# Kernel optimization log

Measured on AMD Instinct MI355X. Metric: run time of the kernel, lower is better.

## Reference

```python
import jax, jax.numpy as jnp
import numpy as np

B, S, D, H, O = 256, 64, 256, 1024, 512
N_CELLS = 3


def setup_inputs() -> dict:
    key = jax.random.key(0)
    ks = jax.random.split(key, 16)

    def u(k, shape, fan):
        return (jax.random.uniform(k, shape, jnp.float32, -1.0, 1.0) / np.float32(np.sqrt(fan)))

    inp = {"inputs": jax.random.normal(ks[0], (B, S, D), jnp.float32)}
    in_dims = [D, H, H]
    i = 1
    for c in range(N_CELLS):
        inp[f"w_ih_{c}"] = u(ks[i], (3 * H, in_dims[c]), H); i += 1
        inp[f"w_hh_{c}"] = u(ks[i], (3 * H, H), H); i += 1
        inp[f"b_ih_{c}"] = u(ks[i], (3 * H,), H); i += 1
        inp[f"b_hh_{c}"] = u(ks[i], (3 * H,), H); i += 1
    inp["lin_w"] = u(ks[13], (S, H, O), H)   # per-step linear weights (same_linear=False)
    inp["lin_b"] = u(ks[14], (S, O), H)
    return inp


def _gru_cell(x, h, w_ih, w_hh, b_ih, b_hh):
    # PyTorch GRUCell gate order: r, z, n
    gi = x @ w_ih.T + b_ih          # [B, 3H]
    gh = h @ w_hh.T + b_hh          # [B, 3H]
    i_r, i_z, i_n = jnp.split(gi, 3, axis=-1)
    h_r, h_z, h_n = jnp.split(gh, 3, axis=-1)
    r = jax.nn.sigmoid(i_r + h_r)
    z = jax.nn.sigmoid(i_z + h_z)
    n = jnp.tanh(i_n + r * h_n)
    return (1.0 - z) * n + z * h


def reference(inputs, w_ih_0, w_hh_0, b_ih_0, b_hh_0,
              w_ih_1, w_hh_1, b_ih_1, b_hh_1,
              w_ih_2, w_hh_2, b_ih_2, b_hh_2,
              lin_w, lin_b):
    params = [(w_ih_0, w_hh_0, b_ih_0, b_hh_0),
              (w_ih_1, w_hh_1, b_ih_1, b_hh_1),
              (w_ih_2, w_hh_2, b_ih_2, b_hh_2)]
    batch = inputs.shape[0]
    hdim = w_hh_0.shape[1]

    def step(hs, xs):
        x_t, wL, bL = xs              # [B,D], [H,O], [O]
        new_hs = []
        cur = x_t
        for i, (wi, wh, bi, bh) in enumerate(params):
            h = _gru_cell(cur, hs[i], wi, wh, bi, bh)
            new_hs.append(h)
            cur = h
        out = cur @ wL + bL           # [B,O]
        return tuple(new_hs), out

    h0 = tuple(jnp.zeros((batch, hdim), inputs.dtype) for _ in range(N_CELLS))
    xs = (jnp.swapaxes(inputs, 0, 1), lin_w, lin_b)  # scan over seq dim
    hs, outs = jax.lax.scan(step, h0, xs)            # outs: [S,B,O]
    return (jnp.swapaxes(outs, 0, 1), hs[0], hs[1], hs[2])
```

## Files before the change

kernel.cpp:

```cpp
#include <hip/hip_runtime.h>
#include <hip/hip_bf16.h>
#include <stdint.h>

#define B_ 256
#define S_ 64
#define D_ 256
#define H_ 1024
#define O_ 512
#define G_ 3072
#define BH_ (B_ * H_)
#define RING_ 32

typedef unsigned short u16;
typedef __attribute__((ext_vector_type(8))) short bf16x8;
typedef __attribute__((ext_vector_type(4))) float f32x4;

#define MFMA16(a, b, c) __builtin_amdgcn_mfma_f32_16x16x32_bf16((a), (b), (c), 0, 0, 0)

__device__ __forceinline__ u16 f2b(float f) {
    union { float f; uint32_t u; } v; v.f = f;
    uint32_t u = v.u;
    return (u16)((u + 0x7fffu + ((u >> 16) & 1u)) >> 16);
}

__device__ __forceinline__ void gl_lds16(const u16* g, u16* l) {
    __builtin_amdgcn_global_load_lds(
        (const __attribute__((address_space(1))) unsigned int*)g,
        (__attribute__((address_space(3))) unsigned int*)l, 16, 0, 0);
}
__device__ __forceinline__ unsigned long long sysld64(const u16* p) {
    return __hip_atomic_load((const unsigned long long*)p, __ATOMIC_RELAXED, __HIP_MEMORY_SCOPE_SYSTEM);
}
__device__ __forceinline__ void sysst64(u16* p, unsigned long long v) {
    __hip_atomic_store((unsigned long long*)p, v, __ATOMIC_RELAXED, __HIP_MEMORY_SCOPE_SYSTEM);
}
__device__ __forceinline__ void waitflag(int* f, int n) {
    while (__hip_atomic_load(f, __ATOMIC_RELAXED, __HIP_MEMORY_SCOPE_SYSTEM) < n)
        __builtin_amdgcn_s_sleep(8);
    asm volatile("" ::: "memory");
}
__device__ __forceinline__ void postflag(int* f) {
    __hip_atomic_fetch_add(f, 1, __ATOMIC_RELAXED, __HIP_MEMORY_SCOPE_SYSTEM);
}


__global__ void k_conv(const float* __restrict__ s, u16* __restrict__ d, int n4) {
    int i = blockIdx.x * blockDim.x + threadIdx.x;
    int st = gridDim.x * blockDim.x;
    for (; i < n4; i += st) {
        float4 v = ((const float4*)s)[i];
        ushort4 o;
        o.x = f2b(v.x); o.y = f2b(v.y); o.z = f2b(v.z); o.w = f2b(v.w);
        ((ushort4*)d)[i] = o;
    }
}

__global__ __launch_bounds__(256) void k_twl(const float* __restrict__ w, u16* __restrict__ o) {
    __shared__ float tile[32][33];
    int bid = blockIdx.x;
    int t = bid >> 9;
    int rem = bid & 511;
    int j0 = (rem >> 4) << 5;
    int o0 = (rem & 15) << 5;
    int tx = threadIdx.x & 31, ty = threadIdx.x >> 5;
    const float* base = w + (size_t)t * (H_ * O_);
#pragma unroll
    for (int i = 0; i < 4; ++i) {
        int r = ty + (i << 3);
        tile[r][tx] = base[(size_t)(j0 + r) * O_ + o0 + tx];
    }
    __syncthreads();
    u16* ob = o + (size_t)t * (O_ * H_);
#pragma unroll
    for (int i = 0; i < 4; ++i) {
        int r = ty + (i << 3);
        ob[(size_t)(o0 + r) * H_ + j0 + tx] = f2b(tile[tx][r]);
    }
}


struct GruArgs {
    const u16* Xb;
    const u16 *Wi0, *Wh0, *Wi1, *Wh1, *Wi2, *Wh2;
    const float *bi0, *bh0, *bi1, *bh1, *bi2, *bh2;
    u16 *h0, *h1, *h2a;
    const u16* WLt;
    const float* lb;
    float* out;
    int* ready;
    int* consumed;
};

__global__ __launch_bounds__(512, 1) void k_gru(GruArgs p) {
    __shared__ u16 Wb[2][3][128 * 64];
    __shared__ u16 Ab[2][32 * 64];
    __shared__ float carry[32 * 132];

    const int w = blockIdx.x;
    const int xcd = w & 7;
    const int slot = w >> 3;
    const int role = slot >> 3;
    const int sub = slot & 7;
    const int b0 = sub * 32;

    const int tid = threadIdx.x;
    const int wid = tid >> 6, lane = tid & 63;
    const int fr = lane & 15, kc = lane >> 4;

    const int arow = tid >> 4;
    const int acol = (tid & 15) << 2;
    const int adst = arow * 64 + ((((tid & 15) >> 1) ^ (arow & 7)) << 3) + ((tid & 1) << 2);

    int sw0 = ((kc ^ (fr & 7)) << 3);
    int sw1 = (((4 + kc) ^ (fr & 7)) << 3);

    int* ready = p.ready;
    int* consumed = p.consumed;

    for (int i = tid; i < 32 * 132; i += 512) carry[i] = 0.f;
    __syncthreads();

    if (role < 3) {
        const u16 *Wi, *Wh; const float *bi, *bh; int K0;
        if (role == 0)      { Wi = p.Wi0; Wh = p.Wh0; bi = p.bi0; bh = p.bh0; K0 = D_; }
        else if (role == 1) { Wi = p.Wi1; Wh = p.Wh1; bi = p.bi1; bh = p.bh1; K0 = H_; }
        else                { Wi = p.Wi2; Wh = p.Wh2; bi = p.bi2; bh = p.bh2; K0 = H_; }
        const int nXc = K0 >> 6;
        const int nC = nXc + 16;
        const int j0 = xcd * 128;
        const int jme = j0 + (wid << 4) + fr;
        const float b_r = bi[jme] + bh[jme];
        const float b_z = bi[H_ + jme] + bh[H_ + jme];
        const float b_i = bi[2 * H_ + jme];
        const float b_h = bh[2 * H_ + jme];

        const u16 *A0 = nullptr, *Ah = nullptr; int ld0 = H_;
        u16* hout = nullptr;

        auto LA = [&](int c) -> unsigned long long {
            const u16* s = (c < nXc) ? (A0 + (size_t)arow * ld0 + (c << 6) + acol)
                                     : (Ah + (size_t)arow * H_ + ((c - nXc) << 6) + acol);
            return sysld64(s);
        };
        auto SW = [&](int c, int nb) {
            if (c < nXc) {
                int ko = c << 6;
#pragma unroll
                for (int hh = 0; hh < 2; ++hh) {
                    int ci = (hh << 9) + tid, jr = ci >> 3, c8 = ci & 7;
                    size_t ro = (size_t)(j0 + jr) * K0 + ko + ((c8 ^ (jr & 7)) << 3);
                    gl_lds16(Wi + ro,                       &Wb[nb][0][ci << 3]);
                    gl_lds16(Wi + (size_t)H_ * K0 + ro,     &Wb[nb][1][ci << 3]);
                    gl_lds16(Wi + (size_t)2 * H_ * K0 + ro, &Wb[nb][2][ci << 3]);
                }
            } else {
                int ko = (c - nXc) << 6;
#pragma unroll
                for (int hh = 0; hh < 2; ++hh) {
                    int ci = (hh << 9) + tid, jr = ci >> 3, c8 = ci & 7;
                    size_t ro = (size_t)(j0 + jr) * H_ + ko + ((c8 ^ (jr & 7)) << 3);
                    gl_lds16(Wh + ro,                       &Wb[nb][0][ci << 3]);
                    gl_lds16(Wh + (size_t)H_ * H_ + ro,     &Wb[nb][1][ci << 3]);
                    gl_lds16(Wh + (size_t)2 * H_ * H_ + ro, &Wb[nb][2][ci << 3]);
                }
            }
        };

        for (int t = 0; t < S_; ++t) {
            if (role == 0) {
                if (t) waitflag(&ready[0 * 64 + t - 1], 64);
                A0 = p.Xb + (size_t)b0 * (S_ * D_) + t * D_; ld0 = S_ * D_;
                Ah = p.h0 + (size_t)((t + RING_ - 1) & (RING_ - 1)) * BH_ + (size_t)b0 * H_;
                hout = p.h0 + (size_t)(t & (RING_ - 1)) * BH_;
            } else if (role == 1) {
                waitflag(&ready[0 * 64 + t], 64);
                if (t) waitflag(&ready[1 * 64 + t - 1], 64);
                A0 = p.h0 + (size_t)(t & (RING_ - 1)) * BH_ + (size_t)b0 * H_; ld0 = H_;
                Ah = p.h1 + (size_t)((t + RING_ - 1) & (RING_ - 1)) * BH_ + (size_t)b0 * H_;
                hout = p.h1 + (size_t)(t & (RING_ - 1)) * BH_;
            } else {
                waitflag(&ready[1 * 64 + t], 64);
                if (t) waitflag(&ready[2 * 64 + t - 1], 64);
                A0 = p.h1 + (size_t)(t & (RING_ - 1)) * BH_ + (size_t)b0 * H_; ld0 = H_;
                Ah = p.h2a + (size_t)t * BH_ + (size_t)b0 * H_;
                hout = p.h2a + (size_t)(t + 1) * BH_;
            }

            f32x4 accR[2] = {}, accZ[2] = {}, accI[2] = {}, accN[2] = {};

            unsigned long long la0 = LA(0), la1 = LA(1);
            *(unsigned long long*)&Ab[0][adst] = la0;
            SW(0, 0);
            la0 = LA(2);

            auto BODY = [&](int s, unsigned long long& laReg) {
                if (s + 2 < nC) asm volatile("s_waitcnt vmcnt(1)" ::: "memory");
                else            asm volatile("s_waitcnt vmcnt(0)" ::: "memory");
                asm volatile("s_waitcnt lgkmcnt(0)" ::: "memory");
                __builtin_amdgcn_s_barrier();
                __builtin_amdgcn_sched_barrier(0);
                if (s + 1 < nC) {
                    *(unsigned long long*)&Ab[(s + 1) & 1][adst] = laReg;
                    SW(s + 1, (s + 1) & 1);
                }
                if (s + 3 < nC) laReg = LA(s + 3);
                const int cur = s & 1;
                const int bo = ((wid << 4) + fr) * 64;
                bf16x8 a00 = *(const bf16x8*)&Ab[cur][fr * 64 + sw0];
                bf16x8 a01 = *(const bf16x8*)&Ab[cur][fr * 64 + sw1];
                bf16x8 a10 = *(const bf16x8*)&Ab[cur][(16 + fr) * 64 + sw0];
                bf16x8 a11 = *(const bf16x8*)&Ab[cur][(16 + fr) * 64 + sw1];
                bf16x8 r0 = *(const bf16x8*)&Wb[cur][0][bo + sw0];
                bf16x8 r1 = *(const bf16x8*)&Wb[cur][0][bo + sw1];
                bf16x8 z0 = *(const bf16x8*)&Wb[cur][1][bo + sw0];
                bf16x8 z1 = *(const bf16x8*)&Wb[cur][1][bo + sw1];
                bf16x8 q0 = *(const bf16x8*)&Wb[cur][2][bo + sw0];
                bf16x8 q1 = *(const bf16x8*)&Wb[cur][2][bo + sw1];
                __builtin_amdgcn_s_setprio(1);
                accR[0] = MFMA16(a00, r0, accR[0]); accR[0] = MFMA16(a01, r1, accR[0]);
                accR[1] = MFMA16(a10, r0, accR[1]); accR[1] = MFMA16(a11, r1, accR[1]);
                accZ[0] = MFMA16(a00, z0, accZ[0]); accZ[0] = MFMA16(a01, z1, accZ[0]);
                accZ[1] = MFMA16(a10, z0, accZ[1]); accZ[1] = MFMA16(a11, z1, accZ[1]);
                if (s < nXc) {
                    accI[0] = MFMA16(a00, q0, accI[0]); accI[0] = MFMA16(a01, q1, accI[0]);
                    accI[1] = MFMA16(a10, q0, accI[1]); accI[1] = MFMA16(a11, q1, accI[1]);
                } else {
                    accN[0] = MFMA16(a00, q0, accN[0]); accN[0] = MFMA16(a01, q1, accN[0]);
                    accN[1] = MFMA16(a10, q0, accN[1]); accN[1] = MFMA16(a11, q1, accN[1]);
                }
                __builtin_amdgcn_s_setprio(0);
            };
            for (int s = 0; s < nC; s += 2) { BODY(s, la1); BODY(s + 1, la0); }

            if (role <= 1 && t >= RING_) waitflag(&consumed[role * 64 + (t - RING_)], 128);

            u16* hrep = &Wb[0][0][0];
#pragma unroll
            for (int m = 0; m < 2; ++m)
#pragma unroll
                for (int i = 0; i < 4; ++i) {
                    int row = m * 16 + kc * 4 + i;
                    float rv = 1.f / (1.f + __expf(-(accR[m][i] + b_r)));
                    float zv = 1.f / (1.f + __expf(-(accZ[m][i] + b_z)));
                    float nv = tanhf(accI[m][i] + b_i + rv * (accN[m][i] + b_h));
                    float hp = carry[row * 132 + (wid << 4) + fr];
                    float hn = (1.f - zv) * nv + zv * hp;
                    carry[row * 132 + (wid << 4) + fr] = hn;
                    hrep[row * 128 + (wid << 4) + fr] = f2b(hn);
                }
            __syncthreads();
            {
                int rr = tid >> 4, jo = (tid & 15) << 3;
                unsigned long long v0 = *(const unsigned long long*)&hrep[rr * 128 + jo];
                unsigned long long v1 = *(const unsigned long long*)&hrep[rr * 128 + jo + 4];
                u16* dst = hout + (size_t)(b0 + rr) * H_ + j0 + jo;
                sysst64(dst, v0);
                sysst64(dst + 4, v1);
            }
            if (t == S_ - 1) {
                int rr = tid >> 4, jo = (tid & 15) << 3;
                float* od = p.out + (size_t)B_ * S_ * O_ + (size_t)role * BH_ +
                            (size_t)(b0 + rr) * H_ + j0 + jo;
                *(float4*)od       = *(const float4*)&carry[rr * 132 + jo];
                *(float4*)(od + 4) = *(const float4*)&carry[rr * 132 + jo + 4];
            }
            asm volatile("s_waitcnt vmcnt(0)" ::: "memory");
            __syncthreads();
            if (tid == 0) {
                postflag(&ready[role * 64 + t]);
                if (role == 0) { if (t) postflag(&consumed[0 * 64 + t - 1]); }
                else if (role == 1) {
                    postflag(&consumed[0 * 64 + t]);
                    if (t) postflag(&consumed[1 * 64 + t - 1]);
                } else {
                    postflag(&consumed[1 * 64 + t]);
                }
            }
            __syncthreads();
        }
    } else {
        const int o0 = xcd << 6;
        const int nC = 16;
        const int mg = wid >> 2, og = wid & 3;
        const u16 *A0 = nullptr, *Wl = nullptr;

        auto LAl = [&](int c) -> unsigned long long {
            return sysld64(A0 + (size_t)arow * H_ + (c << 6) + acol);
        };
        auto SWl = [&](int c, int nb) {
            int orow = tid >> 3, c8 = tid & 7;
            gl_lds16(Wl + (size_t)(o0 + orow) * H_ + (c << 6) + ((c8 ^ (orow & 7)) << 3),
                     &Wb[nb][0][tid << 3]);
        };

        for (int t = 0; t < S_; ++t) {
            waitflag(&ready[2 * 64 + t], 64);
            A0 = p.h2a + (size_t)(t + 1) * BH_ + (size_t)b0 * H_;
            Wl = p.WLt + (size_t)t * (O_ * H_);

            f32x4 acc = {0.f, 0.f, 0.f, 0.f};
            unsigned long long la0 = LAl(0), la1 = LAl(1);
            *(unsigned long long*)&Ab[0][adst] = la0;
            SWl(0, 0);
            la0 = LAl(2);

            auto BODYL = [&](int s, unsigned long long& laReg) {
                if (s + 2 < nC) asm volatile("s_waitcnt vmcnt(1)" ::: "memory");
                else            asm volatile("s_waitcnt vmcnt(0)" ::: "memory");
                asm volatile("s_waitcnt lgkmcnt(0)" ::: "memory");
                __builtin_amdgcn_s_barrier();
                __builtin_amdgcn_sched_barrier(0);
                if (s + 1 < nC) {
                    *(unsigned long long*)&Ab[(s + 1) & 1][adst] = laReg;
                    SWl(s + 1, (s + 1) & 1);
                }
                if (s + 3 < nC) laReg = LAl(s + 3);
                const int cur = s & 1;
                bf16x8 a0 = *(const bf16x8*)&Ab[cur][(mg * 16 + fr) * 64 + sw0];
                bf16x8 a1 = *(const bf16x8*)&Ab[cur][(mg * 16 + fr) * 64 + sw1];
                bf16x8 w0 = *(const bf16x8*)&Wb[cur][0][(og * 16 + fr) * 64 + sw0];
                bf16x8 w1 = *(const bf16x8*)&Wb[cur][0][(og * 16 + fr) * 64 + sw1];
                __builtin_amdgcn_s_setprio(1);
                acc = MFMA16(a0, w0, acc);
                acc = MFMA16(a1, w1, acc);
                __builtin_amdgcn_s_setprio(0);
            };
            for (int s = 0; s < nC; s += 2) { BODYL(s, la1); BODYL(s + 1, la0); }

            float bb = p.lb[t * O_ + o0 + og * 16 + fr];
#pragma unroll
            for (int i = 0; i < 4; ++i) {
                int row = mg * 16 + kc * 4 + i;
                p.out[((size_t)(b0 + row) * S_ + t) * O_ + o0 + og * 16 + fr] = acc[i] + bb;
            }
        }
    }
}


extern "C" void kernel_launch(void* const* d_in, const int* in_sizes, int n_in,
                              void* d_out, int out_size, void* d_ws, size_t ws_size,
                              hipStream_t stream) {
    (void)in_sizes; (void)n_in; (void)out_size; (void)ws_size;
    const float* x   = (const float*)d_in[0];
    const float* wi0 = (const float*)d_in[1];
    const float* wh0 = (const float*)d_in[2];
    const float* bi0 = (const float*)d_in[3];
    const float* bh0 = (const float*)d_in[4];
    const float* wi1 = (const float*)d_in[5];
    const float* wh1 = (const float*)d_in[6];
    const float* bi1 = (const float*)d_in[7];
    const float* bh1 = (const float*)d_in[8];
    const float* wi2 = (const float*)d_in[9];
    const float* wh2 = (const float*)d_in[10];
    const float* bi2 = (const float*)d_in[11];
    const float* bh2 = (const float*)d_in[12];
    const float* lw  = (const float*)d_in[13];
    const float* lb  = (const float*)d_in[14];

    char* base = (char*)d_ws;
    size_t off = 0;
    auto alloc = [&](size_t bytes) {
        char* p = base + off;
        off = (off + bytes + 255) & ~(size_t)255;
        return p;
    };
    u16* Xb  = (u16*)alloc((size_t)B_ * S_ * D_ * 2);
    u16* Wi0 = (u16*)alloc((size_t)G_ * D_ * 2);
    u16* Wh0 = (u16*)alloc((size_t)G_ * H_ * 2);
    u16* Wi1 = (u16*)alloc((size_t)G_ * H_ * 2);
    u16* Wh1 = (u16*)alloc((size_t)G_ * H_ * 2);
    u16* Wi2 = (u16*)alloc((size_t)G_ * H_ * 2);
    u16* Wh2 = (u16*)alloc((size_t)G_ * H_ * 2);
    u16* h0  = (u16*)alloc((size_t)RING_ * BH_ * 2);
    u16* h1  = (u16*)alloc((size_t)RING_ * BH_ * 2);
    u16* h2a = (u16*)alloc((size_t)(S_ + 1) * BH_ * 2);
    u16* WLt = (u16*)alloc((size_t)S_ * O_ * H_ * 2);
    int* flags = (int*)alloc((size_t)(3 * 64 + 2 * 64) * 4);
    int* ready = flags;
    int* consumed = flags + 3 * 64;

    k_conv<<<1024, 256, 0, stream>>>(x,   Xb,  (B_ * S_ * D_) / 4);
    k_conv<<<1024, 256, 0, stream>>>(wi0, Wi0, (G_ * D_) / 4);
    k_conv<<<1024, 256, 0, stream>>>(wh0, Wh0, (G_ * H_) / 4);
    k_conv<<<1024, 256, 0, stream>>>(wi1, Wi1, (G_ * H_) / 4);
    k_conv<<<1024, 256, 0, stream>>>(wh1, Wh1, (G_ * H_) / 4);
    k_conv<<<1024, 256, 0, stream>>>(wi2, Wi2, (G_ * H_) / 4);
    k_conv<<<1024, 256, 0, stream>>>(wh2, Wh2, (G_ * H_) / 4);
    k_twl<<<S_ * 512, 256, 0, stream>>>(lw, WLt);
    hipMemsetAsync(h0 + (size_t)(RING_ - 1) * BH_, 0, (size_t)BH_ * 2, stream);
    hipMemsetAsync(h1 + (size_t)(RING_ - 1) * BH_, 0, (size_t)BH_ * 2, stream);
    hipMemsetAsync(h2a, 0, (size_t)BH_ * 2, stream);
    hipMemsetAsync(flags, 0, (size_t)(3 * 64 + 2 * 64) * 4, stream);

    GruArgs ga;
    ga.Xb = Xb;
    ga.Wi0 = Wi0; ga.Wh0 = Wh0; ga.Wi1 = Wi1; ga.Wh1 = Wh1; ga.Wi2 = Wi2; ga.Wh2 = Wh2;
    ga.bi0 = bi0; ga.bh0 = bh0; ga.bi1 = bi1; ga.bh1 = bh1; ga.bi2 = bi2; ga.bh2 = bh2;
    ga.h0 = h0; ga.h1 = h1; ga.h2a = h2a;
    ga.WLt = WLt; ga.lb = lb; ga.out = (float*)d_out;
    ga.ready = ready; ga.consumed = consumed;

    void* args[] = {&ga};
    hipLaunchCooperativeKernel((void*)k_gru, dim3(256), dim3(512), args, 0, stream);
}
```

Measured before the change: 2.615 ms.

## Triple-buffer weight tiles, use sc0 sc1 loads, keep hidden carry in registers

```diff
diff --git a/kernel.cpp b/kernel.cpp
--- a/kernel.cpp
+++ b/kernel.cpp
@@ -28,11 +28,15 @@
         (const __attribute__((address_space(1))) unsigned int*)g,
         (__attribute__((address_space(3))) unsigned int*)l, 16, 0, 0);
 }
-__device__ __forceinline__ unsigned long long sysld64(const u16* p) {
-    return __hip_atomic_load((const unsigned long long*)p, __ATOMIC_RELAXED, __HIP_MEMORY_SCOPE_SYSTEM);
-}
-__device__ __forceinline__ void sysst64(u16* p, unsigned long long v) {
-    __hip_atomic_store((unsigned long long*)p, v, __ATOMIC_RELAXED, __HIP_MEMORY_SCOPE_SYSTEM);
+__device__ __forceinline__ unsigned long long gld_sys(const u16* p) {
+    unsigned long long v;
+    asm volatile("global_load_dwordx2 %0, %1, off sc0 sc1"
+                 : "=v"(v) : "v"(p) : "memory");
+    return v;
+}
+__device__ __forceinline__ void gst_sys(u16* p, unsigned long long v) {
+    asm volatile("global_store_dwordx2 %0, %1, off sc0 sc1"
+                 :: "v"(p), "v"(v) : "memory");
 }
 __device__ __forceinline__ void waitflag(int* f, int n) {
     while (__hip_atomic_load(f, __ATOMIC_RELAXED, __HIP_MEMORY_SCOPE_SYSTEM) < n)
@@ -92,9 +96,8 @@
 };
 
 __global__ __launch_bounds__(512, 1) void k_gru(GruArgs p) {
-    __shared__ u16 Wb[2][3][128 * 64];
+    __shared__ u16 Wb[3][3][128 * 64];
     __shared__ u16 Ab[2][32 * 64];
-    __shared__ float carry[32 * 132];
 
     const int w = blockIdx.x;
     const int xcd = w & 7;
@@ -116,9 +119,6 @@
 
     int* ready = p.ready;
     int* consumed = p.consumed;
-
-    for (int i = tid; i < 32 * 132; i += 512) carry[i] = 0.f;
-    __syncthreads();
 
     if (role < 3) {
         const u16 *Wi, *Wh; const float *bi, *bh; int K0;
@@ -137,10 +137,12 @@
         const u16 *A0 = nullptr, *Ah = nullptr; int ld0 = H_;
         u16* hout = nullptr;
 
+        f32x4 hcar[2] = {};
+
         auto LA = [&](int c) -> unsigned long long {
             const u16* s = (c < nXc) ? (A0 + (size_t)arow * ld0 + (c << 6) + acol)
                                      : (Ah + (size_t)arow * H_ + ((c - nXc) << 6) + acol);
-            return sysld64(s);
+            return gld_sys(s);
         };
         auto SW = [&](int c, int nb) {
             if (c < nXc) {
@@ -188,49 +190,55 @@
 
             f32x4 accR[2] = {}, accZ[2] = {}, accI[2] = {}, accN[2] = {};
 
-            unsigned long long la0 = LA(0), la1 = LA(1);
-            *(unsigned long long*)&Ab[0][adst] = la0;
             SW(0, 0);
-            la0 = LA(2);
+            unsigned long long la_t = LA(0);
+            unsigned long long r1 = LA(1);
+            unsigned long long r0 = LA(2);
+            SW(1, 1);
+            asm volatile("s_waitcnt vmcnt(8)" ::: "memory");
+            *(unsigned long long*)&Ab[0][adst] = la_t;
+            asm volatile("s_waitcnt lgkmcnt(0)" ::: "memory");
+            __builtin_amdgcn_sched_barrier(0);
 
             auto BODY = [&](int s, unsigned long long& laReg) {
-                if (s + 2 < nC) asm volatile("s_waitcnt vmcnt(1)" ::: "memory");
+                if (s + 2 < nC) asm volatile("s_waitcnt vmcnt(7)" ::: "memory");
                 else            asm volatile("s_waitcnt vmcnt(0)" ::: "memory");
-                asm volatile("s_waitcnt lgkmcnt(0)" ::: "memory");
                 __builtin_amdgcn_s_barrier();
                 __builtin_amdgcn_sched_barrier(0);
-                if (s + 1 < nC) {
-                    *(unsigned long long*)&Ab[(s + 1) & 1][adst] = laReg;
-                    SW(s + 1, (s + 1) & 1);
-                }
+                if (s + 1 < nC) *(unsigned long long*)&Ab[(s + 1) & 1][adst] = laReg;
                 if (s + 3 < nC) laReg = LA(s + 3);
+                if (s + 2 < nC) SW(s + 2, (s + 2) % 3);
+                __builtin_amdgcn_sched_barrier(0);
                 const int cur = s & 1;
+                const int wcur = s % 3;
                 const int bo = ((wid << 4) + fr) * 64;
                 bf16x8 a00 = *(const bf16x8*)&Ab[cur][fr * 64 + sw0];
                 bf16x8 a01 = *(const bf16x8*)&Ab[cur][fr * 64 + sw1];
                 bf16x8 a10 = *(const bf16x8*)&Ab[cur][(16 + fr) * 64 + sw0];
                 bf16x8 a11 = *(const bf16x8*)&Ab[cur][(16 + fr) * 64 + sw1];
-                bf16x8 r0 = *(const bf16x8*)&Wb[cur][0][bo + sw0];
-                bf16x8 r1 = *(const bf16x8*)&Wb[cur][0][bo + sw1];
-                bf16x8 z0 = *(const bf16x8*)&Wb[cur][1][bo + sw0];
-                bf16x8 z1 = *(const bf16x8*)&Wb[cur][1][bo + sw1];
-                bf16x8 q0 = *(const bf16x8*)&Wb[cur][2][bo + sw0];
-                bf16x8 q1 = *(const bf16x8*)&Wb[cur][2][bo + sw1];
+                bf16x8 rr0 = *(const bf16x8*)&Wb[wcur][0][bo + sw0];
+                bf16x8 rr1 = *(const bf16x8*)&Wb[wcur][0][bo + sw1];
+                bf16x8 zz0 = *(const bf16x8*)&Wb[wcur][1][bo + sw0];
+                bf16x8 zz1 = *(const bf16x8*)&Wb[wcur][1][bo + sw1];
+                bf16x8 qq0 = *(const bf16x8*)&Wb[wcur][2][bo + sw0];
+                bf16x8 qq1 = *(const bf16x8*)&Wb[wcur][2][bo + sw1];
+                asm volatile("s_waitcnt lgkmcnt(0)" ::: "memory");
+                __builtin_amdgcn_sched_barrier(0);
                 __builtin_amdgcn_s_setprio(1);
-                accR[0] = MFMA16(a00, r0, accR[0]); accR[0] = MFMA16(a01, r1, accR[0]);
-                accR[1] = MFMA16(a10, r0, accR[1]); accR[1] = MFMA16(a11, r1, accR[1]);
-                accZ[0] = MFMA16(a00, z0, accZ[0]); accZ[0] = MFMA16(a01, z1, accZ[0]);
-                accZ[1] = MFMA16(a10, z0, accZ[1]); accZ[1] = MFMA16(a11, z1, accZ[1]);
+                accR[0] = MFMA16(a00, rr0, accR[0]); accR[0] = MFMA16(a01, rr1, accR[0]);
+                accR[1] = MFMA16(a10, rr0, accR[1]); accR[1] = MFMA16(a11, rr1, accR[1]);
+                accZ[0] = MFMA16(a00, zz0, accZ[0]); accZ[0] = MFMA16(a01, zz1, accZ[0]);
+                accZ[1] = MFMA16(a10, zz0, accZ[1]); accZ[1] = MFMA16(a11, zz1, accZ[1]);
                 if (s < nXc) {
-                    accI[0] = MFMA16(a00, q0, accI[0]); accI[0] = MFMA16(a01, q1, accI[0]);
-                    accI[1] = MFMA16(a10, q0, accI[1]); accI[1] = MFMA16(a11, q1, accI[1]);
+                    accI[0] = MFMA16(a00, qq0, accI[0]); accI[0] = MFMA16(a01, qq1, accI[0]);
+                    accI[1] = MFMA16(a10, qq0, accI[1]); accI[1] = MFMA16(a11, qq1, accI[1]);
                 } else {
-                    accN[0] = MFMA16(a00, q0, accN[0]); accN[0] = MFMA16(a01, q1, accN[0]);
-                    accN[1] = MFMA16(a10, q0, accN[1]); accN[1] = MFMA16(a11, q1, accN[1]);
+                    accN[0] = MFMA16(a00, qq0, accN[0]); accN[0] = MFMA16(a01, qq1, accN[0]);
+                    accN[1] = MFMA16(a10, qq0, accN[1]); accN[1] = MFMA16(a11, qq1, accN[1]);
                 }
                 __builtin_amdgcn_s_setprio(0);
             };
-            for (int s = 0; s < nC; s += 2) { BODY(s, la1); BODY(s + 1, la0); }
+            for (int s = 0; s < nC; s += 2) { BODY(s, r1); BODY(s + 1, r0); }
 
             if (role <= 1 && t >= RING_) waitflag(&consumed[role * 64 + (t - RING_)], 128);
 
@@ -243,9 +251,8 @@
                     float rv = 1.f / (1.f + __expf(-(accR[m][i] + b_r)));
                     float zv = 1.f / (1.f + __expf(-(accZ[m][i] + b_z)));
                     float nv = tanhf(accI[m][i] + b_i + rv * (accN[m][i] + b_h));
-                    float hp = carry[row * 132 + (wid << 4) + fr];
-                    float hn = (1.f - zv) * nv + zv * hp;
-                    carry[row * 132 + (wid << 4) + fr] = hn;
+                    float hn = (1.f - zv) * nv + zv * hcar[m][i];
+                    hcar[m][i] = hn;
                     hrep[row * 128 + (wid << 4) + fr] = f2b(hn);
                 }
             __syncthreads();
@@ -254,15 +261,18 @@
                 unsigned long long v0 = *(const unsigned long long*)&hrep[rr * 128 + jo];
                 unsigned long long v1 = *(const unsigned long long*)&hrep[rr * 128 + jo + 4];
                 u16* dst = hout + (size_t)(b0 + rr) * H_ + j0 + jo;
-                sysst64(dst, v0);
-                sysst64(dst + 4, v1);
+                gst_sys(dst, v0);
+                gst_sys(dst + 4, v1);
             }
             if (t == S_ - 1) {
-                int rr = tid >> 4, jo = (tid & 15) << 3;
-                float* od = p.out + (size_t)B_ * S_ * O_ + (size_t)role * BH_ +
-                            (size_t)(b0 + rr) * H_ + j0 + jo;
-                *(float4*)od       = *(const float4*)&carry[rr * 132 + jo];
-                *(float4*)(od + 4) = *(const float4*)&carry[rr * 132 + jo + 4];
+                float* ob = p.out + (size_t)B_ * S_ * O_ + (size_t)role * BH_;
+#pragma unroll
+                for (int m = 0; m < 2; ++m)
+#pragma unroll
+                    for (int i = 0; i < 4; ++i) {
+                        int row = m * 16 + kc * 4 + i;
+                        ob[(size_t)(b0 + row) * H_ + jme] = hcar[m][i];
+                    }
             }
             asm volatile("s_waitcnt vmcnt(0)" ::: "memory");
             __syncthreads();
@@ -285,7 +295,7 @@
         const u16 *A0 = nullptr, *Wl = nullptr;
 
         auto LAl = [&](int c) -> unsigned long long {
-            return sysld64(A0 + (size_t)arow * H_ + (c << 6) + acol);
+            return gld_sys(A0 + (size_t)arow * H_ + (c << 6) + acol);
         };
         auto SWl = [&](int c, int nb) {
             int orow = tid >> 3, c8 = tid & 7;
@@ -299,33 +309,39 @@
             Wl = p.WLt + (size_t)t * (O_ * H_);
 
             f32x4 acc = {0.f, 0.f, 0.f, 0.f};
-            unsigned long long la0 = LAl(0), la1 = LAl(1);
-            *(unsigned long long*)&Ab[0][adst] = la0;
             SWl(0, 0);
-            la0 = LAl(2);
+            unsigned long long la_t = LAl(0);
+            unsigned long long r1 = LAl(1);
+            unsigned long long r0 = LAl(2);
+            SWl(1, 1);
+            asm volatile("s_waitcnt vmcnt(3)" ::: "memory");
+            *(unsigned long long*)&Ab[0][adst] = la_t;
+            asm volatile("s_waitcnt lgkmcnt(0)" ::: "memory");
+            __builtin_amdgcn_sched_barrier(0);
 
             auto BODYL = [&](int s, unsigned long long& laReg) {
-                if (s + 2 < nC) asm volatile("s_waitcnt vmcnt(1)" ::: "memory");
+                if (s + 2 < nC) asm volatile("s_waitcnt vmcnt(2)" ::: "memory");
                 else            asm volatile("s_waitcnt vmcnt(0)" ::: "memory");
-                asm volatile("s_waitcnt lgkmcnt(0)" ::: "memory");
                 __builtin_amdgcn_s_barrier();
                 __builtin_amdgcn_sched_barrier(0);
-                if (s + 1 < nC) {
-                    *(unsigned long long*)&Ab[(s + 1) & 1][adst] = laReg;
-                    SWl(s + 1, (s + 1) & 1);
-                }
+                if (s + 1 < nC) *(unsigned long long*)&Ab[(s + 1) & 1][adst] = laReg;
                 if (s + 3 < nC) laReg = LAl(s + 3);
+                if (s + 2 < nC) SWl(s + 2, (s + 2) % 3);
+                __builtin_amdgcn_sched_barrier(0);
                 const int cur = s & 1;
+                const int wcur = s % 3;
                 bf16x8 a0 = *(const bf16x8*)&Ab[cur][(mg * 16 + fr) * 64 + sw0];
                 bf16x8 a1 = *(const bf16x8*)&Ab[cur][(mg * 16 + fr) * 64 + sw1];
-                bf16x8 w0 = *(const bf16x8*)&Wb[cur][0][(og * 16 + fr) * 64 + sw0];
-                bf16x8 w1 = *(const bf16x8*)&Wb[cur][0][(og * 16 + fr) * 64 + sw1];
+                bf16x8 w0 = *(const bf16x8*)&Wb[wcur][0][(og * 16 + fr) * 64 + sw0];
+                bf16x8 w1 = *(const bf16x8*)&Wb[wcur][0][(og * 16 + fr) * 64 + sw1];
+                asm volatile("s_waitcnt lgkmcnt(0)" ::: "memory");
+                __builtin_amdgcn_sched_barrier(0);
                 __builtin_amdgcn_s_setprio(1);
                 acc = MFMA16(a0, w0, acc);
                 acc = MFMA16(a1, w1, acc);
                 __builtin_amdgcn_s_setprio(0);
             };
-            for (int s = 0; s < nC; s += 2) { BODYL(s, la1); BODYL(s + 1, la0); }
+            for (int s = 0; s < nC; s += 2) { BODYL(s, r1); BODYL(s + 1, r0); }
 
             float bb = p.lb[t * O_ + o0 + og * 16 + fr];
 #pragma unroll
```

Result: faster. 2.395 ms (-8.4%).
